# Kernel tuning notes

Hardware: AMD Instinct MI355X
Metric: run time of the kernel (lower is better)

## Reference

```python
import jax, jax.numpy as jnp
import numpy as np

B, N = 4096, 8192

def setup_inputs() -> dict:
    key = jax.random.key(0)
    k1, k2 = jax.random.split(key)
    p_target = jax.random.uniform(k1, (B, N), dtype=jnp.float32)
    p_estimate = jax.random.uniform(k2, (B, N), dtype=jnp.float32)
    # normalize to valid probability distributions (as in real MOS data)
    p_target = p_target / p_target.sum(axis=1, keepdims=True)
    p_estimate = p_estimate / p_estimate.sum(axis=1, keepdims=True)
    return {"p_estimate": p_estimate, "p_target": p_target}

def _quantiles(cdf, qs):
    # cdf: [B, N] monotone CDF; qs: [P] percentiles.
    # Find smallest i with cdf[i] >= q, then piecewise-linear interp between
    # (x[i-1], cdf[i-1]) and (x[i], cdf[i]) with x = 1..N; for i==0 the torch
    # code interpolates from (0, 0) to (1, cdf[0]). Segment width is always 1.
    n = cdf.shape[1]
    i = jnp.sum(cdf[:, None, :] < qs[None, :, None], axis=-1)  # [B, P]
    i = jnp.clip(i, 0, n - 1)
    Yb = jnp.take_along_axis(cdf, i, axis=1)                    # cdf[i]
    Ya = jnp.where(i == 0, jnp.zeros((), cdf.dtype),
                   jnp.take_along_axis(cdf, jnp.maximum(i - 1, 0), axis=1))
    # Xb = i+1, slope A = (Yb - Ya) / 1; score = Xb + (q - Yb) / A
    return (i + 1).astype(cdf.dtype) + (qs[None, :] - Yb) / (Yb - Ya)

def reference(p_estimate, p_target):
    qs = jnp.array([0.25, 0.5, 0.75], dtype=p_target.dtype)
    quan1 = _quantiles(jnp.cumsum(p_target, axis=1), qs)   # [B, 3]
    quan2 = _quantiles(jnp.cumsum(p_estimate, axis=1), qs)  # [B, 3]
    return jnp.mean(jnp.abs(quan1 - quan2))
```

## Files before the change

### kernel.cpp

```cpp
#include <hip/hip_runtime.h>


constexpr int BLOCK = 256;
constexpr int CHUNK = 32;
constexpr int NCOL  = 8192;

__global__ __launch_bounds__(BLOCK) void row_quantiles(
    const float* __restrict__ pe, const float* __restrict__ pt,
    float* __restrict__ qe, float* __restrict__ qt)
{
    const float* src = (blockIdx.y == 0) ? pe : pt;
    float*       dst = (blockIdx.y == 0) ? qe : qt;
    const int row = blockIdx.x;
    const int tid = threadIdx.x;
    const float* rp = src + (size_t)row * NCOL + (size_t)tid * CHUNK;

    float v[CHUNK];
    #pragma unroll
    for (int k = 0; k < CHUNK / 4; ++k) {
        const float4 f = *reinterpret_cast<const float4*>(rp + 4 * k);
        v[4*k+0] = f.x; v[4*k+1] = f.y; v[4*k+2] = f.z; v[4*k+3] = f.w;
    }
    float lsum = 0.f;
    #pragma unroll
    for (int k = 0; k < CHUNK; ++k) lsum += v[k];

    const int lane = tid & 63, wave = tid >> 6;
    float x = lsum;
    #pragma unroll
    for (int off = 1; off < 64; off <<= 1) {
        const float y = __shfl_up(x, off, 64);
        if (lane >= off) x += y;
    }
    __shared__ float wsum[4];
    __shared__ float sbase[BLOCK + 1];
    __shared__ float qscore[3];
    if (lane == 63) wsum[wave] = x;
    __syncthreads();
    float wbase = 0.f;
    #pragma unroll
    for (int w = 0; w < 4; ++w) if (w < wave) wbase += wsum[w];
    float excl = __shfl_up(x, 1, 64);
    if (lane == 0) excl = 0.f;
    sbase[tid] = wbase + excl;
    if (tid == BLOCK - 1) sbase[BLOCK] = wbase + x;
    __syncthreads();

    const float base  = sbase[tid];
    const float nbase = sbase[tid + 1];
    const float qs[3] = {0.25f, 0.5f, 0.75f};
    #pragma unroll
    for (int qi = 0; qi < 3; ++qi) {
        const float q = qs[qi];
        const bool owner = (base < q && nbase >= q) ||
                           (tid == BLOCK - 1 && nbase < q);
        if (owner) {
            float run = base, prev = base;
            float Yb = 0.f, Ya = 0.f;
            int idx = -1;
            #pragma unroll
            for (int k = 0; k < CHUNK; ++k) {
                prev = run;
                run += v[k];
                if (idx < 0 && run >= q) { idx = k; Yb = run; Ya = prev; }
            }
            if (idx < 0) { idx = CHUNK - 1; Yb = run; Ya = prev; }
            const float score = (float)(tid * CHUNK + idx + 1) + (q - Yb) / (Yb - Ya);
            qscore[qi] = score;
        }
    }
    __syncthreads();
    if (tid < 3) dst[row * 3 + tid] = qscore[tid];
}

__global__ __launch_bounds__(256) void reduce_absdiff(
    const float* __restrict__ qe, const float* __restrict__ qt,
    float* __restrict__ out, int n)
{
    const int tid = threadIdx.x;
    float s = 0.f;
    for (int i = tid; i < n; i += 256) s += fabsf(qe[i] - qt[i]);
    #pragma unroll
    for (int off = 32; off > 0; off >>= 1) s += __shfl_down(s, off, 64);
    __shared__ float ws[4];
    if ((tid & 63) == 0) ws[tid >> 6] = s;
    __syncthreads();
    if (tid == 0) out[0] = (ws[0] + ws[1] + ws[2] + ws[3]) / (float)n;
}

extern "C" void kernel_launch(void* const* d_in, const int* in_sizes, int n_in,
                              void* d_out, int out_size, void* d_ws, size_t ws_size,
                              hipStream_t stream) {
    const float* pe = (const float*)d_in[0];
    const float* pt = (const float*)d_in[1];
    const int B = in_sizes[0] / NCOL;
    float* qe = (float*)d_ws;
    float* qt = qe + (size_t)B * 3;
    dim3 grid(B, 2);
    row_quantiles<<<grid, BLOCK, 0, stream>>>(pe, pt, qe, qt);
    reduce_absdiff<<<1, 256, 0, stream>>>(qe, qt, (float*)d_out, B * 3);
}
```

Before: 57.89 us.

## Fuse quantile and reduction into one kernel with atomic accumulation

Merges the per-row quantile kernel and the single-block reduction into one kernel. Each block handles both matrices for its row, accumulates the abs diff, and atomically adds the result to the output after a memset. The load layout changes to coalesced float4 segments with group sums kept in shared memory, and the owning group's float4 is re-read from global memory instead of held in registers. This removes the second launch and the serial reduction, at the cost of a memset, atomic contention on one address, and the two matrices being processed one after the other within each block.

```diff
diff --git a/kernel.cpp b/kernel.cpp
--- a/kernel.cpp
+++ b/kernel.cpp
@@ -2,90 +2,96 @@
 
 
 constexpr int BLOCK = 256;
-constexpr int CHUNK = 32;
 constexpr int NCOL  = 8192;
+constexpr int NSEG  = NCOL / (4 * BLOCK);
+constexpr int NGRP  = NCOL / 4;
 
-__global__ __launch_bounds__(BLOCK) void row_quantiles(
+__global__ __launch_bounds__(BLOCK) void mquantile_fused(
     const float* __restrict__ pe, const float* __restrict__ pt,
-    float* __restrict__ qe, float* __restrict__ qt)
+    float* __restrict__ out, float inv_total)
 {
-    const float* src = (blockIdx.y == 0) ? pe : pt;
-    float*       dst = (blockIdx.y == 0) ? qe : qt;
-    const int row = blockIdx.x;
-    const int tid = threadIdx.x;
-    const float* rp = src + (size_t)row * NCOL + (size_t)tid * CHUNK;
+    __shared__ float b[NGRP + 1];
+    __shared__ float wsum[4];
+    __shared__ float qsc[2][3];
+    const int row  = blockIdx.x;
+    const int tid  = threadIdx.x;
+    const int lane = tid & 63, wave = tid >> 6;
+    const float qs[3] = {0.25f, 0.5f, 0.75f};
 
-    float v[CHUNK];
-    #pragma unroll
-    for (int k = 0; k < CHUNK / 4; ++k) {
-        const float4 f = *reinterpret_cast<const float4*>(rp + 4 * k);
-        v[4*k+0] = f.x; v[4*k+1] = f.y; v[4*k+2] = f.z; v[4*k+3] = f.w;
+    for (int m = 0; m < 2; ++m) {
+        const float* rp = (m == 0 ? pe : pt) + (size_t)row * NCOL;
+
+        #pragma unroll
+        for (int s = 0; s < NSEG; ++s) {
+            const float4 v = *reinterpret_cast<const float4*>(rp + s * 1024 + tid * 4);
+            b[s * BLOCK + tid] = v.x + v.y + v.z + v.w;
+        }
+        __syncthreads();
+
+        float g[8];
+        float lsum = 0.f;
+        #pragma unroll
+        for (int j = 0; j < 8; ++j) { g[j] = b[tid * 8 + j]; lsum += g[j]; }
+
+        float x = lsum;
+        #pragma unroll
+        for (int off = 1; off < 64; off <<= 1) {
+            const float y = __shfl_up(x, off, 64);
+            if (lane >= off) x += y;
+        }
+        if (lane == 63) wsum[wave] = x;
+        __syncthreads();
+
+        float wbase = 0.f;
+        #pragma unroll
+        for (int w = 0; w < 4; ++w) if (w < wave) wbase += wsum[w];
+        float excl = __shfl_up(x, 1, 64);
+        if (lane == 0) excl = 0.f;
+        float run = wbase + excl;
+        #pragma unroll
+        for (int j = 0; j < 8; ++j) { b[tid * 8 + j] = run; run += g[j]; }
+        if (tid == BLOCK - 1) b[NGRP] = run;
+        __syncthreads();
+
+        float b0[NSEG], b1[NSEG];
+        #pragma unroll
+        for (int s = 0; s < NSEG; ++s) {
+            b0[s] = b[s * BLOCK + tid];
+            b1[s] = b[s * BLOCK + tid + 1];
+        }
+        const float total = b[NGRP];
+        #pragma unroll
+        for (int qi = 0; qi < 3; ++qi) {
+            const float q = qs[qi];
+            #pragma unroll
+            for (int s = 0; s < NSEG; ++s) {
+                const int gi = s * BLOCK + tid;
+                const bool owner = (b0[s] < q && b1[s] >= q) ||
+                                   (gi == NGRP - 1 && total < q);
+                if (owner) {
+                    const float4 v = *reinterpret_cast<const float4*>(rp + s * 1024 + tid * 4);
+                    const float vv[4] = {v.x, v.y, v.z, v.w};
+                    float runw = b0[s], prev = b0[s], Yb = 0.f, Ya = 0.f;
+                    int idx = -1;
+                    #pragma unroll
+                    for (int c = 0; c < 4; ++c) {
+                        prev = runw; runw += vv[c];
+                        if (idx < 0 && runw >= q) { idx = c; Yb = runw; Ya = prev; }
+                    }
+                    if (idx < 0) { idx = 3; Yb = runw; Ya = prev; }
+                    qsc[m][qi] = (float)(gi * 4 + idx + 1) + (q - Yb) / (Yb - Ya);
+                }
+            }
+        }
+        __syncthreads();
     }
-    float lsum = 0.f;
-    #pragma unroll
-    for (int k = 0; k < CHUNK; ++k) lsum += v[k];
 
-    const int lane = tid & 63, wave = tid >> 6;
-    float x = lsum;
-    #pragma unroll
-    for (int off = 1; off < 64; off <<= 1) {
-        const float y = __shfl_up(x, off, 64);
-        if (lane >= off) x += y;
+    if (tid == 0) {
+        const float s = fabsf(qsc[0][0] - qsc[1][0]) +
+                        fabsf(qsc[0][1] - qsc[1][1]) +
+                        fabsf(qsc[0][2] - qsc[1][2]);
+        atomicAdd(out, s * inv_total);
     }
-    __shared__ float wsum[4];
-    __shared__ float sbase[BLOCK + 1];
-    __shared__ float qscore[3];
-    if (lane == 63) wsum[wave] = x;
-    __syncthreads();
-    float wbase = 0.f;
-    #pragma unroll
-    for (int w = 0; w < 4; ++w) if (w < wave) wbase += wsum[w];
-    float excl = __shfl_up(x, 1, 64);
-    if (lane == 0) excl = 0.f;
-    sbase[tid] = wbase + excl;
-    if (tid == BLOCK - 1) sbase[BLOCK] = wbase + x;
-    __syncthreads();
-
-    const float base  = sbase[tid];
-    const float nbase = sbase[tid + 1];
-    const float qs[3] = {0.25f, 0.5f, 0.75f};
-    #pragma unroll
-    for (int qi = 0; qi < 3; ++qi) {
-        const float q = qs[qi];
-        const bool owner = (base < q && nbase >= q) ||
-                           (tid == BLOCK - 1 && nbase < q);
-        if (owner) {
-            float run = base, prev = base;
-            float Yb = 0.f, Ya = 0.f;
-            int idx = -1;
-            #pragma unroll
-            for (int k = 0; k < CHUNK; ++k) {
-                prev = run;
-                run += v[k];
-                if (idx < 0 && run >= q) { idx = k; Yb = run; Ya = prev; }
-            }
-            if (idx < 0) { idx = CHUNK - 1; Yb = run; Ya = prev; }
-            const float score = (float)(tid * CHUNK + idx + 1) + (q - Yb) / (Yb - Ya);
-            qscore[qi] = score;
-        }
-    }
-    __syncthreads();
-    if (tid < 3) dst[row * 3 + tid] = qscore[tid];
-}
-
-__global__ __launch_bounds__(256) void reduce_absdiff(
-    const float* __restrict__ qe, const float* __restrict__ qt,
-    float* __restrict__ out, int n)
-{
-    const int tid = threadIdx.x;
-    float s = 0.f;
-    for (int i = tid; i < n; i += 256) s += fabsf(qe[i] - qt[i]);
-    #pragma unroll
-    for (int off = 32; off > 0; off >>= 1) s += __shfl_down(s, off, 64);
-    __shared__ float ws[4];
-    if ((tid & 63) == 0) ws[tid >> 6] = s;
-    __syncthreads();
-    if (tid == 0) out[0] = (ws[0] + ws[1] + ws[2] + ws[3]) / (float)n;
 }
 
 extern "C" void kernel_launch(void* const* d_in, const int* in_sizes, int n_in,
@@ -94,9 +100,7 @@
     const float* pe = (const float*)d_in[0];
     const float* pt = (const float*)d_in[1];
     const int B = in_sizes[0] / NCOL;
-    float* qe = (float*)d_ws;
-    float* qt = qe + (size_t)B * 3;
-    dim3 grid(B, 2);
-    row_quantiles<<<grid, BLOCK, 0, stream>>>(pe, pt, qe, qt);
-    reduce_absdiff<<<1, 256, 0, stream>>>(qe, qt, (float*)d_out, B * 3);
+    hipMemsetAsync(d_out, 0, sizeof(float), stream);
+    mquantile_fused<<<B, BLOCK, 0, stream>>>(pe, pt, (float*)d_out,
+                                             1.0f / (3.0f * (float)B));
 }
```

After: 78.96 us. +36.4%, slower.
